# Kernel tuning notes

Hardware: AMD Instinct MI355X
Metric: run time of the kernel (lower is better)

The kernel has to match this reference:

```python
import jax, jax.numpy as jnp
import numpy as np

N_NODES = 50000
N_EDGES = 800000
D_IN = 64
D_HID = 64
N_LAYERS = 3
BN_EPS = 1e-5


def setup_inputs() -> dict:
    key = jax.random.key(0)
    ks = jax.random.split(key, 10)
    x = jax.random.normal(ks[0], (N_NODES, D_IN), dtype=jnp.float32)
    edge_index = jax.random.randint(ks[1], (2, N_EDGES), 0, N_NODES, dtype=jnp.int32)
    # Per-layer GCN weights (in==hid==64 so we can stack) and BatchNorm params.
    Ws = jax.random.normal(ks[2], (N_LAYERS, D_HID, D_HID), dtype=jnp.float32) / np.sqrt(D_HID)
    bs = jnp.zeros((N_LAYERS, D_HID), dtype=jnp.float32)
    gammas = jnp.ones((N_LAYERS, D_HID), dtype=jnp.float32)
    betas = jnp.zeros((N_LAYERS, D_HID), dtype=jnp.float32)
    means = jax.random.normal(ks[3], (N_LAYERS, D_HID), dtype=jnp.float32) * 0.1
    variances = jax.random.uniform(ks[4], (N_LAYERS, D_HID), dtype=jnp.float32, minval=0.5, maxval=1.5)
    lin_w = jax.random.normal(ks[5], (D_HID, 1), dtype=jnp.float32) / np.sqrt(D_HID)
    lin_b = jnp.zeros((1,), dtype=jnp.float32)
    return {"x": x, "edge_index": edge_index, "Ws": Ws, "bs": bs,
            "gammas": gammas, "betas": betas, "means": means,
            "variances": variances, "lin_w": lin_w, "lin_b": lin_b}


def _gnn_forward(x, edge_index, Ws, bs, gammas, betas, means, variances, lin_w, lin_b):
    n = x.shape[0]
    # GCNConv: add self loops, symmetric D^{-1/2}(A+I)D^{-1/2} normalization.
    loop = jnp.arange(n, dtype=edge_index.dtype)
    row = jnp.concatenate([edge_index[0], loop])  # source nodes
    col = jnp.concatenate([edge_index[1], loop])  # target nodes
    deg = jax.ops.segment_sum(jnp.ones(row.shape[0], x.dtype), col, num_segments=n)
    dinv = jax.lax.rsqrt(jnp.maximum(deg, 1.0))  # deg >= 1 from self loops
    norm = (dinv[row] * dinv[col])[:, None]  # [E+N, 1]

    h = x
    for i in range(N_LAYERS):
        h = h @ Ws[i]  # transform first (PyG GCNConv order)
        h = jax.ops.segment_sum(h[row] * norm, col, num_segments=n) + bs[i]
        # BatchNorm1d (eval mode: running stats) + ReLU; dropout is identity in eval.
        h = (h - means[i]) * jax.lax.rsqrt(variances[i] + BN_EPS) * gammas[i] + betas[i]
        h = jax.nn.relu(h)
    out = h @ lin_w + lin_b  # [N, 1]
    return out[:, 0]


def reference(x, edge_index, Ws, bs, gammas, betas, means, variances, lin_w, lin_b):
    return _gnn_forward(x, edge_index, Ws, bs, gammas, betas, means, variances, lin_w, lin_b)
```

## Files before the change

### kernel.cpp

```cpp
#include <hip/hip_runtime.h>
#include <hip/hip_bf16.h>
#include <hip/hip_fp16.h>


#define BN_EPS 1e-5f
#define CAP 64
#define CHUNK 4096
#define SEGCAP 5120
#define NBINS_MAX 256

typedef _Float16 f16x8 __attribute__((ext_vector_type(8)));
typedef float f32x4 __attribute__((ext_vector_type(4)));

__global__ __launch_bounds__(256) void k_bin_pairs(const int* __restrict__ row,
                                                   const int* __restrict__ col,
                                                   int* __restrict__ gfill,
                                                   unsigned int* __restrict__ gpairs,
                                                   int e, int nbins) {
    __shared__ unsigned int pl[CHUNK];
    __shared__ int bcnt[NBINS_MAX];
    __shared__ int bbase[NBINS_MAX];
    int tid = threadIdx.x;
    int base = blockIdx.x * CHUNK;
    for (int b = tid; b < nbins; b += 256) bcnt[b] = 0;
    __syncthreads();
    int nloc = e - base; if (nloc > CHUNK) nloc = CHUNK;
    #pragma unroll
    for (int it = 0; it < CHUNK / 1024; ++it) {
        int le = (it * 256 + tid) * 4;
        if (le + 3 < nloc) {
            int i4 = (base >> 2) + it * 256 + tid;
            int4 r = ((const int4*)row)[i4];
            int4 c = ((const int4*)col)[i4];
            atomicAdd(&bcnt[c.x >> 8], 1); pl[le + 0] = (unsigned)r.x | ((unsigned)c.x << 16);
            atomicAdd(&bcnt[c.y >> 8], 1); pl[le + 1] = (unsigned)r.y | ((unsigned)c.y << 16);
            atomicAdd(&bcnt[c.z >> 8], 1); pl[le + 2] = (unsigned)r.z | ((unsigned)c.z << 16);
            atomicAdd(&bcnt[c.w >> 8], 1); pl[le + 3] = (unsigned)r.w | ((unsigned)c.w << 16);
        } else {
            for (int j = 0; j < 4; ++j) {
                if (le + j < nloc) {
                    int rr = row[base + le + j];
                    int cc = col[base + le + j];
                    atomicAdd(&bcnt[cc >> 8], 1);
                    pl[le + j] = (unsigned)rr | ((unsigned)cc << 16);
                }
            }
        }
    }
    __syncthreads();
    for (int b = tid; b < nbins; b += 256) {
        bbase[b] = atomicAdd(&gfill[b], bcnt[b]);
        bcnt[b] = 0;
    }
    __syncthreads();
    for (int i = tid; i < nloc; i += 256) {
        unsigned int p = pl[i];
        int bin = p >> 24;
        int off = atomicAdd(&bcnt[bin], 1);
        int pos = bbase[bin] + off;
        if (pos < SEGCAP) gpairs[(size_t)bin * SEGCAP + pos] = p;
    }
}

__global__ __launch_bounds__(256) void k_bucket_build(const unsigned int* __restrict__ gpairs,
                                                      const int* __restrict__ gfill,
                                                      int* __restrict__ cnt,
                                                      unsigned short* __restrict__ bucket,
                                                      int n) {
    __shared__ unsigned short lb[256 * CAP];
    __shared__ int lc[256];
    int tid = threadIdx.x;
    int bin = blockIdx.x;
    lc[tid] = 0;
    __syncthreads();
    int m = gfill[bin]; if (m > SEGCAP) m = SEGCAP;
    const unsigned int* seg = gpairs + (size_t)bin * SEGCAP;
    for (int i = tid; i < m; i += 256) {
        unsigned int p = seg[i];
        int src = p & 0xffff;
        int dl = (p >> 16) & 255;
        int pos = atomicAdd(&lc[dl], 1);
        if (pos < CAP) lb[dl * CAP + pos] = (unsigned short)src;
    }
    __syncthreads();
    int nodebase = bin << 8;
    const int4* lb4 = (const int4*)lb;
    int4* gb4 = (int4*)bucket;
    for (int i = tid; i < 256 * 8; i += 256) {
        int rrow = i >> 3;
        int gnode = nodebase + rrow;
        if (gnode < n) gb4[(size_t)gnode * 8 + (i & 7)] = lb4[i];
    }
    int gnode = nodebase + tid;
    if (gnode < n) cnt[gnode] = lc[tid];
}

__global__ __launch_bounds__(256) void k_wprep(const float* __restrict__ Ws,
                                               __half* __restrict__ wt) {
    int l = blockIdx.x;
    int tid = threadIdx.x;
    const float* W = Ws + l * 4096;
    __half* hi = wt + (size_t)l * 8192;
    __half* lo = hi + 4096;
    for (int i = tid; i < 4096; i += 256) {
        int k = i >> 6, nn = i & 63;
        float w = W[k * 64 + nn];
        __half h = __float2half_rn(w);
        hi[nn * 64 + k] = h;
        lo[nn * 64 + k] = __float2half_rn(w - __half2float(h));
    }
}

template<bool L0>
__global__ __launch_bounds__(256) void k_mm_mfma(const void* __restrict__ Ain,
                                                 const __half* __restrict__ wt,
                                                 const int* __restrict__ cnt,
                                                 __half* __restrict__ out, int n) {
    int tid = threadIdx.x;
    int w = tid >> 6;
    int lane = tid & 63;
    int r = lane & 15;
    int kg = lane >> 4;
    int row = blockIdx.x * 64 + w * 16 + r;
    bool inb = row < n;

    f16x8 ahi0 = {}, ahi1 = {}, alo0 = {}, alo1 = {};
    if (L0) {
        const float* A = (const float*)Ain;
        if (inb) {
            float di = rsqrtf((float)(cnt[row] + 1));
            const float4* ap0 = (const float4*)(A + (size_t)row * 64 + kg * 8);
            const float4* ap1 = (const float4*)(A + (size_t)row * 64 + 32 + kg * 8);
            float4 v0 = ap0[0], v1 = ap0[1];
            float4 v2 = ap1[0], v3 = ap1[1];
            float f[16] = {v0.x, v0.y, v0.z, v0.w, v1.x, v1.y, v1.z, v1.w,
                           v2.x, v2.y, v2.z, v2.w, v3.x, v3.y, v3.z, v3.w};
            #pragma unroll
            for (int i = 0; i < 8; ++i) {
                float s0 = f[i] * di, s1 = f[8 + i] * di;
                _Float16 h0 = (_Float16)s0, h1 = (_Float16)s1;
                ahi0[i] = h0; ahi1[i] = h1;
                alo0[i] = (_Float16)(s0 - (float)h0);
                alo1[i] = (_Float16)(s1 - (float)h1);
            }
        }
    } else {
        const __half* A = (const __half*)Ain;
        if (inb) {
            union { uint4 u; f16x8 h; } u0, u1;
            u0.u = *(const uint4*)(A + (size_t)row * 64 + kg * 8);
            u1.u = *(const uint4*)(A + (size_t)row * 64 + 32 + kg * 8);
            ahi0 = u0.h; ahi1 = u1.h;
        }
    }

    const __half* whi = wt;
    const __half* wlo = wt + 4096;
    f32x4 acc[4];
    #pragma unroll
    for (int t = 0; t < 4; ++t) {
        int cb = t * 16 + r;
        union { uint4 u; f16x8 h; } bh0, bh1, bl0, bl1;
        bh0.u = *(const uint4*)(whi + cb * 64 + kg * 8);
        bh1.u = *(const uint4*)(whi + cb * 64 + 32 + kg * 8);
        bl0.u = *(const uint4*)(wlo + cb * 64 + kg * 8);
        bl1.u = *(const uint4*)(wlo + cb * 64 + 32 + kg * 8);
        f32x4 a = {0.f, 0.f, 0.f, 0.f};
        a = __builtin_amdgcn_mfma_f32_16x16x32_f16(ahi0, bh0.h, a, 0, 0, 0);
        a = __builtin_amdgcn_mfma_f32_16x16x32_f16(ahi1, bh1.h, a, 0, 0, 0);
        a = __builtin_amdgcn_mfma_f32_16x16x32_f16(ahi0, bl0.h, a, 0, 0, 0);
        a = __builtin_amdgcn_mfma_f32_16x16x32_f16(ahi1, bl1.h, a, 0, 0, 0);
        if (L0) {
            a = __builtin_amdgcn_mfma_f32_16x16x32_f16(alo0, bh0.h, a, 0, 0, 0);
            a = __builtin_amdgcn_mfma_f32_16x16x32_f16(alo1, bh1.h, a, 0, 0, 0);
        }
        acc[t] = a;
    }

    int orow_base = blockIdx.x * 64 + w * 16 + 4 * kg;
    #pragma unroll
    for (int t = 0; t < 4; ++t) {
        #pragma unroll
        for (int i = 0; i < 4; ++i) {
            int orow = orow_base + i;
            if (orow < n) out[(size_t)orow * 64 + t * 16 + r] = __float2half_rn(acc[t][i]);
        }
    }
}

template<int LAYER, bool FINAL>
__global__ __launch_bounds__(256, 5) void k_agg(const __half* __restrict__ t,
                                                const int* __restrict__ cnt,
                                                const unsigned short* __restrict__ bucket,
                                                const float* __restrict__ bias,
                                                const float* __restrict__ gamma,
                                                const float* __restrict__ beta,
                                                const float* __restrict__ mean,
                                                const float* __restrict__ var,
                                                __half* __restrict__ hout,
                                                const float* __restrict__ lw,
                                                const float* __restrict__ lb,
                                                float* __restrict__ outp, int n) {
    int lane = threadIdx.x & 63;
    int g = lane >> 3;
    int q = lane & 7;
    int qo = q << 3;
    float S[8], O[8], LW[8];
    #pragma unroll
    for (int i = 0; i < 8; ++i) {
        int f = qo + i;
        float s = gamma[f] * rsqrtf(var[f] + BN_EPS);
        S[i] = s;
        O[i] = fmaf(bias[f] - mean[f], s, beta[f]);
        if (FINAL) LW[i] = lw[f];
    }
    int wave = (blockIdx.x * blockDim.x + threadIdx.x) >> 6;
    int nwaves = (gridDim.x * blockDim.x) >> 6;
    union HV { float4 f4; __half2 h2[4]; };
    int node = wave;
    int c_pf = 0, idx_pf = 0;
    if (node < n) {
        c_pf = cnt[node];
        idx_pf = (int)bucket[(size_t)node * CAP + lane];
    }
    for (; node < n; node += nwaves) {
        int c = c_pf;
        int myidx = idx_pf;
        HV vself;
        vself.f4 = *(const float4*)(t + ((size_t)node << 6) + qo);
        int nn = node + nwaves;
        if (nn < n) {
            c_pf = cnt[nn];
            idx_pf = (int)bucket[(size_t)nn * CAP + lane];
        }
        int cm1 = c - 1; if (cm1 < 0) cm1 = 0;
        int i1 = __shfl(myidx, (g < cm1 ? g : cm1), 64);
        int i2 = __shfl(myidx, (8 + g < cm1 ? 8 + g : cm1), 64);
        HV v1, v2, v3, v4;
        v1.f4 = *(const float4*)(t + ((size_t)i1 << 6) + qo);
        v2.f4 = *(const float4*)(t + ((size_t)i2 << 6) + qo);
        if (c > 16) {
            int i3 = __shfl(myidx, (16 + g < cm1 ? 16 + g : cm1), 64);
            int i4 = __shfl(myidx, (24 + g < cm1 ? 24 + g : cm1), 64);
            v3.f4 = *(const float4*)(t + ((size_t)i3 << 6) + qo);
            v4.f4 = *(const float4*)(t + ((size_t)i4 << 6) + qo);
        }
        float acc[8] = {0.f, 0.f, 0.f, 0.f, 0.f, 0.f, 0.f, 0.f};
        for (int sub = 0; sub < c; sub += 32) {
            float m1 = (sub + g < c) ? 1.f : 0.f;
            float m2 = (sub + 8 + g < c) ? 1.f : 0.f;
            #pragma unroll
            for (int p = 0; p < 4; ++p) {
                float2 a = __half22float2(v1.h2[p]);
                float2 b = __half22float2(v2.h2[p]);
                acc[2 * p]     = fmaf(m1, a.x, acc[2 * p]);
                acc[2 * p + 1] = fmaf(m1, a.y, acc[2 * p + 1]);
                acc[2 * p]     = fmaf(m2, b.x, acc[2 * p]);
                acc[2 * p + 1] = fmaf(m2, b.y, acc[2 * p + 1]);
            }
            if (sub + 32 < c) {
                int t1 = sub + 32 + g, t2 = sub + 40 + g;
                i1 = __shfl(myidx, (t1 < cm1 ? t1 : cm1), 64);
                i2 = __shfl(myidx, (t2 < cm1 ? t2 : cm1), 64);
                v1.f4 = *(const float4*)(t + ((size_t)i1 << 6) + qo);
                v2.f4 = *(const float4*)(t + ((size_t)i2 << 6) + qo);
            }
            if (sub + 16 < c) {
                float m3 = (sub + 16 + g < c) ? 1.f : 0.f;
                float m4 = (sub + 24 + g < c) ? 1.f : 0.f;
                #pragma unroll
                for (int p = 0; p < 4; ++p) {
                    float2 a = __half22float2(v3.h2[p]);
                    float2 b = __half22float2(v4.h2[p]);
                    acc[2 * p]     = fmaf(m3, a.x, acc[2 * p]);
                    acc[2 * p + 1] = fmaf(m3, a.y, acc[2 * p + 1]);
                    acc[2 * p]     = fmaf(m4, b.x, acc[2 * p]);
                    acc[2 * p + 1] = fmaf(m4, b.y, acc[2 * p + 1]);
                }
            }
            if (sub + 48 < c) {
                int t3 = sub + 48 + g, t4 = sub + 56 + g;
                int i3 = __shfl(myidx, (t3 < cm1 ? t3 : cm1), 64);
                int i4 = __shfl(myidx, (t4 < cm1 ? t4 : cm1), 64);
                v3.f4 = *(const float4*)(t + ((size_t)i3 << 6) + qo);
                v4.f4 = *(const float4*)(t + ((size_t)i4 << 6) + qo);
            }
        }
        {
            float ms = (g == 0) ? 1.f : 0.f;
            #pragma unroll
            for (int p = 0; p < 4; ++p) {
                float2 a = __half22float2(vself.h2[p]);
                acc[2 * p]     = fmaf(ms, a.x, acc[2 * p]);
                acc[2 * p + 1] = fmaf(ms, a.y, acc[2 * p + 1]);
            }
        }
        #pragma unroll
        for (int i = 0; i < 8; ++i) {
            acc[i] += __shfl_down(acc[i], 32, 64);
            acc[i] += __shfl_down(acc[i], 16, 64);
            acc[i] += __shfl_down(acc[i], 8, 64);
        }
        float di = rsqrtf((float)(c + 1));
        if (FINAL) {
            float p = 0.f;
            #pragma unroll
            for (int i = 0; i < 8; ++i) {
                float h = fmaxf(fmaf(acc[i] * di, S[i], O[i]), 0.f);
                p = fmaf(h, LW[i], p);
            }
            p += __shfl_down(p, 4, 64);
            p += __shfl_down(p, 2, 64);
            p += __shfl_down(p, 1, 64);
            if (lane == 0) outp[node] = p + lb[0];
        } else if (g == 0) {
            union { __half2 h2[4]; uint4 u; } o;
            #pragma unroll
            for (int i = 0; i < 4; ++i) {
                float h0 = fmaxf(fmaf(acc[2 * i] * di, S[2 * i], O[2 * i]), 0.f);
                float h1 = fmaxf(fmaf(acc[2 * i + 1] * di, S[2 * i + 1], O[2 * i + 1]), 0.f);
                o.h2[i] = __floats2half2_rn(h0 * di, h1 * di);
            }
            *(uint4*)(hout + ((size_t)node << 6) + qo) = o.u;
        }
    }
}

extern "C" void kernel_launch(void* const* d_in, const int* in_sizes, int n_in,
                              void* d_out, int out_size, void* d_ws, size_t ws_size,
                              hipStream_t stream) {
    const float* x    = (const float*)d_in[0];
    const int*   ei   = (const int*)d_in[1];
    const float* Ws   = (const float*)d_in[2];
    const float* bs   = (const float*)d_in[3];
    const float* gam  = (const float*)d_in[4];
    const float* bet  = (const float*)d_in[5];
    const float* mean = (const float*)d_in[6];
    const float* var  = (const float*)d_in[7];
    const float* lw   = (const float*)d_in[8];
    const float* lb   = (const float*)d_in[9];
    float* out = (float*)d_out;

    const int n = in_sizes[0] / 64;
    const int e = in_sizes[1] / 2;
    const int* row = ei;
    const int* col = ei + e;
    const int nbins = (n + 255) >> 8;

    int* ws_i = (int*)d_ws;
    int* cnt = ws_i;
    int* gfill = ws_i + n;
    unsigned short* bucket = (unsigned short*)(ws_i + n + 256);
    __half* t16 = (__half*)(ws_i + n + 256 + 32 * (size_t)n);
    __half* h16 = t16 + 64 * (size_t)n;
    __half* wt = (__half*)(((uintptr_t)(h16 + 64 * (size_t)n) + 15) & ~(uintptr_t)15);
    unsigned int* gpairs = (unsigned int*)t16;

    int nb_p1 = (e + CHUNK - 1) / CHUNK;
    int nb_mm = (n + 63) / 64;
    int nb_ag = 1280;

    hipMemsetAsync(gfill, 0, 256 * sizeof(int), stream);
    k_wprep<<<3, 256, 0, stream>>>(Ws, wt);
    k_bin_pairs<<<nb_p1, 256, 0, stream>>>(row, col, gfill, gpairs, e, nbins);
    k_bucket_build<<<nbins, 256, 0, stream>>>(gpairs, gfill, cnt, bucket, n);

    k_mm_mfma<true><<<nb_mm, 256, 0, stream>>>(x, wt, cnt, t16, n);
    k_agg<0, false><<<nb_ag, 256, 0, stream>>>(t16, cnt, bucket,
                                               bs, gam, bet, mean, var,
                                               h16, nullptr, nullptr, nullptr, n);
    k_mm_mfma<false><<<nb_mm, 256, 0, stream>>>(h16, wt + 8192, cnt, t16, n);
    k_agg<1, false><<<nb_ag, 256, 0, stream>>>(t16, cnt, bucket,
                                               bs + 64, gam + 64, bet + 64, mean + 64, var + 64,
                                               h16, nullptr, nullptr, nullptr, n);
    k_mm_mfma<false><<<nb_mm, 256, 0, stream>>>(h16, wt + 16384, cnt, t16, n);
    k_agg<2, true><<<nb_ag, 256, 0, stream>>>(t16, cnt, bucket,
                                              bs + 128, gam + 128, bet + 128, mean + 128, var + 128,
                                              nullptr, lw, lb, out, n);
}
```

Measured before the change: 220.1 us.

## Halve CSR bin width, shrink edge chunks, fold weight prep into bucket build

```diff
diff --git a/kernel.cpp b/kernel.cpp
--- a/kernel.cpp
+++ b/kernel.cpp
@@ -5,9 +5,10 @@
 
 #define BN_EPS 1e-5f
 #define CAP 64
-#define CHUNK 4096
-#define SEGCAP 5120
-#define NBINS_MAX 256
+#define CHUNK 2048
+#define BINSH 7
+#define SEGCAP 2560
+#define NBINS_MAX 512
 
 typedef _Float16 f16x8 __attribute__((ext_vector_type(8)));
 typedef float f32x4 __attribute__((ext_vector_type(4)));
@@ -32,16 +33,16 @@
             int i4 = (base >> 2) + it * 256 + tid;
             int4 r = ((const int4*)row)[i4];
             int4 c = ((const int4*)col)[i4];
-            atomicAdd(&bcnt[c.x >> 8], 1); pl[le + 0] = (unsigned)r.x | ((unsigned)c.x << 16);
-            atomicAdd(&bcnt[c.y >> 8], 1); pl[le + 1] = (unsigned)r.y | ((unsigned)c.y << 16);
-            atomicAdd(&bcnt[c.z >> 8], 1); pl[le + 2] = (unsigned)r.z | ((unsigned)c.z << 16);
-            atomicAdd(&bcnt[c.w >> 8], 1); pl[le + 3] = (unsigned)r.w | ((unsigned)c.w << 16);
+            atomicAdd(&bcnt[c.x >> BINSH], 1); pl[le + 0] = (unsigned)r.x | ((unsigned)c.x << 16);
+            atomicAdd(&bcnt[c.y >> BINSH], 1); pl[le + 1] = (unsigned)r.y | ((unsigned)c.y << 16);
+            atomicAdd(&bcnt[c.z >> BINSH], 1); pl[le + 2] = (unsigned)r.z | ((unsigned)c.z << 16);
+            atomicAdd(&bcnt[c.w >> BINSH], 1); pl[le + 3] = (unsigned)r.w | ((unsigned)c.w << 16);
         } else {
             for (int j = 0; j < 4; ++j) {
                 if (le + j < nloc) {
                     int rr = row[base + le + j];
                     int cc = col[base + le + j];
-                    atomicAdd(&bcnt[cc >> 8], 1);
+                    atomicAdd(&bcnt[cc >> BINSH], 1);
                     pl[le + j] = (unsigned)rr | ((unsigned)cc << 16);
                 }
             }
@@ -49,13 +50,14 @@
     }
     __syncthreads();
     for (int b = tid; b < nbins; b += 256) {
-        bbase[b] = atomicAdd(&gfill[b], bcnt[b]);
+        int cb = bcnt[b];
+        bbase[b] = cb ? atomicAdd(&gfill[b], cb) : 0;
         bcnt[b] = 0;
     }
     __syncthreads();
     for (int i = tid; i < nloc; i += 256) {
         unsigned int p = pl[i];
-        int bin = p >> 24;
+        int bin = p >> (16 + BINSH);
         int off = atomicAdd(&bcnt[bin], 1);
         int pos = bbase[bin] + off;
         if (pos < SEGCAP) gpairs[(size_t)bin * SEGCAP + pos] = p;
@@ -66,48 +68,48 @@
                                                       const int* __restrict__ gfill,
                                                       int* __restrict__ cnt,
                                                       unsigned short* __restrict__ bucket,
+                                                      const float* __restrict__ Ws,
+                                                      __half* __restrict__ wt,
                                                       int n) {
-    __shared__ unsigned short lb[256 * CAP];
-    __shared__ int lc[256];
+    __shared__ unsigned short lb[128 * CAP];
+    __shared__ int lc[128];
     int tid = threadIdx.x;
     int bin = blockIdx.x;
-    lc[tid] = 0;
+    if (tid < 128) lc[tid] = 0;
     __syncthreads();
     int m = gfill[bin]; if (m > SEGCAP) m = SEGCAP;
     const unsigned int* seg = gpairs + (size_t)bin * SEGCAP;
     for (int i = tid; i < m; i += 256) {
         unsigned int p = seg[i];
         int src = p & 0xffff;
-        int dl = (p >> 16) & 255;
+        int dl = (p >> 16) & 127;
         int pos = atomicAdd(&lc[dl], 1);
         if (pos < CAP) lb[dl * CAP + pos] = (unsigned short)src;
     }
     __syncthreads();
-    int nodebase = bin << 8;
+    int nodebase = bin << BINSH;
     const int4* lb4 = (const int4*)lb;
     int4* gb4 = (int4*)bucket;
-    for (int i = tid; i < 256 * 8; i += 256) {
+    for (int i = tid; i < 128 * 8; i += 256) {
         int rrow = i >> 3;
         int gnode = nodebase + rrow;
         if (gnode < n) gb4[(size_t)gnode * 8 + (i & 7)] = lb4[i];
     }
-    int gnode = nodebase + tid;
-    if (gnode < n) cnt[gnode] = lc[tid];
-}
-
-__global__ __launch_bounds__(256) void k_wprep(const float* __restrict__ Ws,
-                                               __half* __restrict__ wt) {
-    int l = blockIdx.x;
-    int tid = threadIdx.x;
-    const float* W = Ws + l * 4096;
-    __half* hi = wt + (size_t)l * 8192;
-    __half* lo = hi + 4096;
-    for (int i = tid; i < 4096; i += 256) {
-        int k = i >> 6, nn = i & 63;
-        float w = W[k * 64 + nn];
-        __half h = __float2half_rn(w);
-        hi[nn * 64 + k] = h;
-        lo[nn * 64 + k] = __float2half_rn(w - __half2float(h));
+    if (tid < 128) {
+        int gnode = nodebase + tid;
+        if (gnode < n) cnt[gnode] = lc[tid];
+    }
+    if (bin < 3) {
+        const float* W = Ws + bin * 4096;
+        __half* hi = wt + (size_t)bin * 8192;
+        __half* lo = hi + 4096;
+        for (int i = tid; i < 4096; i += 256) {
+            int k = i >> 6, nn = i & 63;
+            float w = W[k * 64 + nn];
+            __half h = __float2half_rn(w);
+            hi[nn * 64 + k] = h;
+            lo[nn * 64 + k] = __float2half_rn(w - __half2float(h));
+        }
     }
 }
 
@@ -345,13 +347,13 @@
     const int e = in_sizes[1] / 2;
     const int* row = ei;
     const int* col = ei + e;
-    const int nbins = (n + 255) >> 8;
+    const int nbins = (n + (1 << BINSH) - 1) >> BINSH;
 
     int* ws_i = (int*)d_ws;
     int* cnt = ws_i;
     int* gfill = ws_i + n;
-    unsigned short* bucket = (unsigned short*)(ws_i + n + 256);
-    __half* t16 = (__half*)(ws_i + n + 256 + 32 * (size_t)n);
+    unsigned short* bucket = (unsigned short*)(ws_i + n + 512);
+    __half* t16 = (__half*)(ws_i + n + 512 + 32 * (size_t)n);
     __half* h16 = t16 + 64 * (size_t)n;
     __half* wt = (__half*)(((uintptr_t)(h16 + 64 * (size_t)n) + 15) & ~(uintptr_t)15);
     unsigned int* gpairs = (unsigned int*)t16;
@@ -360,10 +362,9 @@
     int nb_mm = (n + 63) / 64;
     int nb_ag = 1280;
 
-    hipMemsetAsync(gfill, 0, 256 * sizeof(int), stream);
-    k_wprep<<<3, 256, 0, stream>>>(Ws, wt);
+    hipMemsetAsync(gfill, 0, NBINS_MAX * sizeof(int), stream);
     k_bin_pairs<<<nb_p1, 256, 0, stream>>>(row, col, gfill, gpairs, e, nbins);
-    k_bucket_build<<<nbins, 256, 0, stream>>>(gpairs, gfill, cnt, bucket, n);
+    k_bucket_build<<<nbins, 256, 0, stream>>>(gpairs, gfill, cnt, bucket, Ws, wt, n);
 
     k_mm_mfma<true><<<nb_mm, 256, 0, stream>>>(x, wt, cnt, t16, n);
     k_agg<0, false><<<nb_ag, 256, 0, stream>>>(t16, cnt, bucket,
```

New measurement: 220.3 us. Within noise of the previous version (+0.1%).
